# Kernel tuning notes

Hardware: AMD Instinct MI355X
Metric: run time of the kernel (lower is better)

## Reference

```python
import jax, jax.numpy as jnp
import numpy as np

T, DB, H, U, MC, MT, L, K = 16, 512, 512, 1024, 8, 4, 64, 64
Hh = H // 2


def setup_inputs() -> dict:
    key = jax.random.key(0)
    ks = jax.random.split(key, 16)
    s = 0.05
    inp = {
        'feat': jax.random.normal(ks[0], (T, DB, H), jnp.float32),
        'key': jax.random.normal(ks[1], (T, H), jnp.float32),
        'final_feature': jax.random.normal(ks[2], (T, L, H), jnp.float32),
        'Wih_f': jax.random.normal(ks[3], (3 * Hh, H), jnp.float32) * s,
        'Whh_f': jax.random.normal(ks[4], (3 * Hh, Hh), jnp.float32) * s,
        'bih_f': jnp.zeros((3 * Hh,), jnp.float32),
        'bhh_f': jnp.zeros((3 * Hh,), jnp.float32),
        'Wih_b': jax.random.normal(ks[5], (3 * Hh, H), jnp.float32) * s,
        'Whh_b': jax.random.normal(ks[6], (3 * Hh, Hh), jnp.float32) * s,
        'bih_b': jnp.zeros((3 * Hh,), jnp.float32),
        'bhh_b': jnp.zeros((3 * Hh,), jnp.float32),
        'Wb': jax.random.normal(ks[7], (H, H), jnp.float32) * s,
        'bb': jnp.zeros((H,), jnp.float32),
        'Kemb': jax.random.normal(ks[8], (K, H), jnp.float32) * s,
        'col_idx': jax.random.randint(ks[9], (U, MC), 0, DB, jnp.int32),
        'col_mask': jax.random.randint(ks[10], (U, MC), 0, 2, jnp.int32).at[:, 0].set(1),
        'tab_idx': jax.random.randint(ks[11], (U, MT), 0, DB, jnp.int32),
        'tab_mask': jax.random.randint(ks[12], (U, MT), 0, 2, jnp.int32).at[:, 0].set(1),
        'attn_mask': jax.random.randint(ks[13], (T, U), 0, 2, jnp.int32).at[:, 0].set(1),
    }
    return inp


def _gru_cell(x, h, Wih, Whh, bih, bhh):
    gi = x @ Wih.T + bih
    gh = h @ Whh.T + bhh
    ir, iz, inn = jnp.split(gi, 3, axis=-1)
    hr, hz, hn = jnp.split(gh, 3, axis=-1)
    r = jax.nn.sigmoid(ir + hr)
    z = jax.nn.sigmoid(iz + hz)
    n = jnp.tanh(inn + r * hn)
    return (1.0 - z) * n + z * h


def reference(feat, key, final_feature, Wih_f, Whh_f, bih_f, bhh_f,
              Wih_b, Whh_b, bih_b, bhh_b, Wb, bb, Kemb,
              col_idx, col_mask, tab_idx, tab_mask, attn_mask):
    # --- irregular gather + masked mean over schema-graph index groups ---
    def masked_mean(idx, m):
        g = feat[:, idx, :]                        # (T, U, M, H) gather
        mf = m.astype(feat.dtype)
        s = jnp.einsum('tumh,um->tuh', g, mf)
        cnt = jnp.maximum(mf.sum(-1), 1.0)         # (U,)
        return s / cnt[None, :, None]

    col_feat = masked_mean(col_idx, col_mask)      # (T, U, H)
    tab_feat = masked_mean(tab_idx, tab_mask)      # (T, U, H)

    # --- bidirectional GRU fuse over the 2-step [table, column] sequence ---
    x1 = tab_feat.reshape(T * U, H)
    x2 = col_feat.reshape(T * U, H)
    h0 = jnp.zeros((T * U, Hh), feat.dtype)
    f1 = _gru_cell(x1, h0, Wih_f, Whh_f, bih_f, bhh_f)
    f2 = _gru_cell(x2, f1, Wih_f, Whh_f, bih_f, bhh_f)
    b1 = _gru_cell(x2, h0, Wih_b, Whh_b, bih_b, bhh_b)
    b2 = _gru_cell(x1, b1, Wih_b, Whh_b, bih_b, bhh_b)
    o0 = jnp.concatenate([f1, b2], axis=-1)        # output at t=0
    o1 = jnp.concatenate([f2, b1], axis=-1)        # output at t=1
    db_emb = ((o0 + o1) * 0.5).reshape(T, U, H)    # mean over seq dim

    # --- attention_sum ---
    logits = jnp.einsum('th,tuh->tu', key, db_emb)
    logits = jnp.where(attn_mask == 0, jnp.asarray(-1e9, logits.dtype), logits)
    w = jax.nn.softmax(logits, axis=-1)
    attn = jnp.einsum('tu,tuh->th', w, db_emb)     # (T, H)

    # --- output_prob with bilinear feature transform ---
    feature = final_feature + attn[:, None, :]     # (T, L, H)
    ff = jnp.tanh(feature @ Wb.T + bb)
    db_prob = jnp.einsum('tlh,tuh->tlu', ff, db_emb)
    kw_prob = jnp.einsum('tlh,kh->tlk', ff, Kemb)
    out = jax.nn.log_softmax(jnp.concatenate([db_prob, kw_prob], axis=-1), axis=-1)
    return out  # (T, L, U+K)
```

## Files before the change

kernel.cpp:

```cpp
#include <hip/hip_runtime.h>
#include <math.h>

#define T_  16
#define DB2_ 512
#define H_  512
#define Hh_ 256
#define U_  1024
#define MC_ 8
#define MT_ 4
#define L_  64
#define K_  64
#define M_  (T_*U_)

#define BM 64
#define BNG 64
#define BK 64
#define S0_ (768*512)
#define S1_ (768*256)
#define WB_ (512*512)
#define KE_ (64*512)

typedef __attribute__((ext_vector_type(8))) short bf16x8;
typedef __attribute__((ext_vector_type(4))) float f32x4;

__device__ __forceinline__ float sigmoidf_(float x) {
    return 1.f / (1.f + __expf(-x));
}
__device__ __forceinline__ float tanhf_(float x) {
    const float xc = fminf(fmaxf(x, -10.f), 10.f);
    const float t = __expf(2.f * xc);
    return (t - 1.f) / (t + 1.f);
}

__device__ __forceinline__ ushort f2bf(float f) {
    union { float f; unsigned u; } v; v.f = f;
    const unsigned r = (v.u + 0x7FFFu + ((v.u >> 16) & 1u)) >> 16;
    return (ushort)r;
}
__device__ __forceinline__ float bf2f(ushort u) {
    union { unsigned u; float f; } v; v.u = ((unsigned)u) << 16; return v.f;
}

__device__ __forceinline__ void gload16(const void* g, void* l) {
    __builtin_amdgcn_global_load_lds(
        (const __attribute__((address_space(1))) void*)g,
        (__attribute__((address_space(3))) void*)l, 16, 0, 0);
}

__global__ __launch_bounds__(256) void wcvt_kernel(
    const float* __restrict__ w0, const float* __restrict__ w1,
    const float* __restrict__ w2, const float* __restrict__ w3,
    const float* __restrict__ w4, const float* __restrict__ w5,
    ushort* __restrict__ dst)
{
    const int idx = (blockIdx.x * 256 + threadIdx.x) * 4;
    const float* src; int local;
    if      (idx < S0_)                  { src = w0; local = idx; }
    else if (idx < S0_ + S1_)            { src = w1; local = idx - S0_; }
    else if (idx < 2*S0_ + S1_)          { src = w2; local = idx - S0_ - S1_; }
    else if (idx < 2*S0_ + 2*S1_)        { src = w3; local = idx - 2*S0_ - S1_; }
    else if (idx < 2*S0_ + 2*S1_ + WB_)  { src = w4; local = idx - 2*S0_ - 2*S1_; }
    else                                 { src = w5; local = idx - 2*S0_ - 2*S1_ - WB_; }
    const float4 v = *(const float4*)(src + local);
    ushort4 o; o.x = f2bf(v.x); o.y = f2bf(v.y); o.z = f2bf(v.z); o.w = f2bf(v.w);
    *(ushort4*)(dst + idx) = o;
}

__global__ __launch_bounds__(256) void meanpool_kernel(
    const float* __restrict__ feat,
    const int* __restrict__ col_idx, const int* __restrict__ col_mask,
    const int* __restrict__ tab_idx, const int* __restrict__ tab_mask,
    ushort* __restrict__ x1, ushort* __restrict__ x2)
{
    const int u = blockIdx.x;
    const int t = blockIdx.y;
    const int tid = threadIdx.x;

    int ci[MC_], cm[MC_], ti[MT_], tm[MT_];
    float cc = 0.f, tc = 0.f;
#pragma unroll
    for (int m = 0; m < MC_; ++m) { ci[m] = col_idx[u*MC_+m]; cm[m] = col_mask[u*MC_+m]; cc += (float)cm[m]; }
#pragma unroll
    for (int m = 0; m < MT_; ++m) { ti[m] = tab_idx[u*MT_+m]; tm[m] = tab_mask[u*MT_+m]; tc += (float)tm[m]; }
    const float rc = 1.f / fmaxf(cc, 1.f);
    const float rt = 1.f / fmaxf(tc, 1.f);

    const float* fb = feat + (size_t)t * DB2_ * H_;
    const int h = tid * 2;

    float acx = 0.f, acy = 0.f, atx = 0.f, aty = 0.f;
#pragma unroll
    for (int m = 0; m < MC_; ++m) if (cm[m]) {
        const float2 v = *(const float2*)(fb + (size_t)ci[m]*H_ + h);
        acx += v.x; acy += v.y;
    }
#pragma unroll
    for (int m = 0; m < MT_; ++m) if (tm[m]) {
        const float2 v = *(const float2*)(fb + (size_t)ti[m]*H_ + h);
        atx += v.x; aty += v.y;
    }
    const size_t o = ((size_t)(t*U_ + u))*H_ + h;
    ushort2 c2; c2.x = f2bf(acx*rc); c2.y = f2bf(acy*rc);
    ushort2 t2; t2.x = f2bf(atx*rt); t2.y = f2bf(aty*rt);
    *(ushort2*)(x2 + o) = c2;
    *(ushort2*)(x1 + o) = t2;
}

template<int GN>
__device__ __forceinline__ void compute_tile64(
    f32x4 (&acc)[4][2][2],
    const ushort (&As)[BM][BK], const ushort (&Bs)[192][BK],
    int lane, int wm, int wn)
{
#pragma unroll
    for (int s = 0; s < 2; ++s) {
        const int colr = (((s*4 + (lane>>4)) ^ (lane & 7)) * 8);
        bf16x8 af[2];
#pragma unroll
        for (int fm = 0; fm < 2; ++fm)
            af[fm] = *(const bf16x8*)&As[wm*32 + fm*16 + (lane&15)][colr];
#pragma unroll
        for (int g = 0; g < 3; ++g) {
            const int gi = (g == 2) ? GN : g;
#pragma unroll
            for (int fn = 0; fn < 2; ++fn) {
                const bf16x8 bv = *(const bf16x8*)&Bs[g*64 + wn*32 + fn*16 + (lane&15)][colr];
#pragma unroll
                for (int fm = 0; fm < 2; ++fm)
                    acc[gi][fm][fn] = __builtin_amdgcn_mfma_f32_16x16x32_bf16(
                        af[fm], bv, acc[gi][fm][fn], 0, 0, 0);
            }
        }
    }
}

template<bool HAS_H>
__global__ __launch_bounds__(256, 4) void gru2_kernel(
    const ushort* __restrict__ X0, const ushort* __restrict__ X1,
    const ushort* __restrict__ Hb0, const ushort* __restrict__ Hb1,
    const ushort* __restrict__ Wih0, const ushort* __restrict__ Wih1,
    const ushort* __restrict__ Whh0, const ushort* __restrict__ Whh1,
    const float* __restrict__ bih0, const float* __restrict__ bih1,
    const float* __restrict__ bhh0, const float* __restrict__ bhh1,
    ushort* __restrict__ HoutB0, ushort* __restrict__ HoutB1,
    ushort* __restrict__ emb0, ushort* __restrict__ emb1)
{
    __shared__ __align__(16) ushort As[BM][BK];
    __shared__ __align__(16) ushort Bs[192][BK];

    const int sel = blockIdx.z;
    const ushort* Xb   = sel ? X1 : X0;
    const ushort* Hb   = sel ? Hb1 : Hb0;
    const ushort* Wihb = sel ? Wih1 : Wih0;
    const ushort* Whhb = sel ? Whh1 : Whh0;
    const float*  bih  = sel ? bih1 : bih0;
    const float*  bhh  = sel ? bhh1 : bhh0;
    ushort* Hout_b = sel ? HoutB1 : HoutB0;
    ushort* emb_b  = sel ? emb1 : emb0;

    const int tid = threadIdx.x;
    const int lane = tid & 63, wid = tid >> 6;
    const int wm = wid >> 1, wn = wid & 1;

    const int flat = blockIdx.x;
    const int i8   = flat & 7;
    const int rest = flat >> 3;
    const int jb   = rest & 3;
    const int ib   = (rest >> 2) * 8 + i8;
    const int i0 = ib * BM;
    const int j0 = jb * BNG;

    const int csw  = (((lane & 7) ^ (lane >> 3)) * 8);
    const int rsub = lane >> 3;

    ushort* const ldsA0 = &As[0][0] + (size_t)wid*512;
    ushort* const ldsA1 = &As[0][0] + (size_t)(wid+4)*512;
    ushort* ldsB[6];
#pragma unroll
    for (int s = 0; s < 6; ++s) ldsB[s] = &Bs[0][0] + (size_t)(wid + 4*s)*512;

    f32x4 acc[4][2][2] = {};

    {
        const ushort* ga0 = Xb + (size_t)(i0 + wid*8     + rsub)*H_ + csw;
        const ushort* ga1 = Xb + (size_t)(i0 + (wid+4)*8 + rsub)*H_ + csw;
        const ushort* gb[6];
#pragma unroll
        for (int s = 0; s < 6; ++s) {
            const int rowB = (wid + 4*s)*8 + rsub;
            gb[s] = Wihb + (size_t)((rowB>>6)*Hh_ + j0 + (rowB&63))*H_ + csw;
        }
        for (int k0 = 0; k0 < H_; k0 += BK) {
            gload16(ga0, ldsA0);
            gload16(ga1, ldsA1);
#pragma unroll
            for (int s = 0; s < 6; ++s) gload16(gb[s], ldsB[s]);
            ga0 += BK; ga1 += BK;
#pragma unroll
            for (int s = 0; s < 6; ++s) gb[s] += BK;
            __syncthreads();
            compute_tile64<2>(acc, As, Bs, lane, wm, wn);
            __syncthreads();
        }
    }
    if (HAS_H) {
        const ushort* ga0 = Hb + (size_t)(i0 + wid*8     + rsub)*Hh_ + csw;
        const ushort* ga1 = Hb + (size_t)(i0 + (wid+4)*8 + rsub)*Hh_ + csw;
        const ushort* gb[6];
#pragma unroll
        for (int s = 0; s < 6; ++s) {
            const int rowB = (wid + 4*s)*8 + rsub;
            gb[s] = Whhb + (size_t)((rowB>>6)*Hh_ + j0 + (rowB&63))*Hh_ + csw;
        }
        for (int k0 = 0; k0 < Hh_; k0 += BK) {
            gload16(ga0, ldsA0);
            gload16(ga1, ldsA1);
#pragma unroll
            for (int s = 0; s < 6; ++s) gload16(gb[s], ldsB[s]);
            ga0 += BK; ga1 += BK;
#pragma unroll
            for (int s = 0; s < 6; ++s) gb[s] += BK;
            __syncthreads();
            compute_tile64<3>(acc, As, Bs, lane, wm, wn);
            __syncthreads();
        }
    }

#pragma unroll
    for (int fn = 0; fn < 2; ++fn) {
        const int j = j0 + wn*32 + fn*16 + (lane & 15);
        const float bri = bih[j],       brh = bhh[j];
        const float bzi = bih[Hh_ + j], bzh = bhh[Hh_ + j];
        const float bni = bih[2*Hh_+j], bnh = bhh[2*Hh_ + j];
#pragma unroll
        for (int fm = 0; fm < 2; ++fm) {
#pragma unroll
            for (int r = 0; r < 4; ++r) {
                const int i = i0 + wm*32 + fm*16 + (lane >> 4)*4 + r;
                const float xr = acc[0][fm][fn][r] + bri + brh;
                const float xz = acc[1][fm][fn][r] + bzi + bzh;
                const float xn = acc[2][fm][fn][r] + bni;
                float hn = bnh, hprev = 0.f;
                if (HAS_H) { hn += acc[3][fm][fn][r]; hprev = bf2f(Hb[(size_t)i*Hh_ + j]); }
                const float rg = sigmoidf_(xr);
                const float zg = sigmoidf_(xz);
                const float ng = tanhf_(xn + rg * hn);
                const float hp = (1.f - zg) * ng + zg * hprev;
                if (HAS_H) {
                    emb_b[(size_t)i*H_ + j] = f2bf(0.5f * (hprev + hp));
                } else {
                    Hout_b[(size_t)i*Hh_ + j] = f2bf(hp);
                }
            }
        }
    }
}

template<int NT>
__device__ __forceinline__ float block_reduce_max(float v, float* red) {
#pragma unroll
    for (int o = 32; o > 0; o >>= 1) v = fmaxf(v, __shfl_down(v, o));
    const int wid = threadIdx.x >> 6;
    if ((threadIdx.x & 63) == 0) red[wid] = v;
    __syncthreads();
    if (threadIdx.x == 0) {
        float m = red[0];
#pragma unroll
        for (int i = 1; i < NT/64; ++i) m = fmaxf(m, red[i]);
        red[0] = m;
    }
    __syncthreads();
    const float r = red[0];
    __syncthreads();
    return r;
}

template<int NT>
__device__ __forceinline__ float block_reduce_sum(float v, float* red) {
#pragma unroll
    for (int o = 32; o > 0; o >>= 1) v += __shfl_down(v, o);
    const int wid = threadIdx.x >> 6;
    if ((threadIdx.x & 63) == 0) red[wid] = v;
    __syncthreads();
    if (threadIdx.x == 0) {
        float m = red[0];
#pragma unroll
        for (int i = 1; i < NT/64; ++i) m += red[i];
        red[0] = m;
    }
    __syncthreads();
    const float r = red[0];
    __syncthreads();
    return r;
}

__global__ __launch_bounds__(256) void attn_logits_kernel(
    const ushort* __restrict__ db, const float* __restrict__ key,
    const int* __restrict__ attn_mask, float* __restrict__ alog)
{
    const int t = blockIdx.y;
    const int tid = threadIdx.x;
    const int u = blockIdx.x*64 + (tid >> 2);
    const int kq = (tid & 3) * 128;

    const bf16x8* r8 = (const bf16x8*)(db + ((size_t)t*U_ + u)*H_ + kq);
    const float* kp = key + t*H_ + kq;
    float s = 0.f;
#pragma unroll
    for (int k8 = 0; k8 < 16; ++k8) {
        const bf16x8 v = r8[k8];
#pragma unroll
        for (int j = 0; j < 8; ++j)
            s = fmaf(kp[k8*8 + j], bf2f((ushort)v[j]), s);
    }
    s += __shfl_xor(s, 1);
    s += __shfl_xor(s, 2);
    if ((tid & 3) == 0)
        alog[t*U_ + u] = attn_mask[t*U_ + u] ? s : -1e9f;
}

__global__ __launch_bounds__(512) void attn_softmax_kernel(
    const float* __restrict__ alog, float* __restrict__ aw)
{
    __shared__ float red[8];
    const int t = blockIdx.x, tid = threadIdx.x;
    const float v0 = alog[t*U_ + tid], v1 = alog[t*U_ + tid + 512];
    const float m = block_reduce_max<512>(fmaxf(v0, v1), red);
    const float e0 = __expf(v0 - m), e1 = __expf(v1 - m);
    const float s = block_reduce_sum<512>(e0 + e1, red);
    const float inv = 1.f / s;
    aw[t*U_ + tid] = e0 * inv;
    aw[t*U_ + tid + 512] = e1 * inv;
}

__global__ __launch_bounds__(512) void attn_wsum_kernel(
    const ushort* __restrict__ db, const float* __restrict__ aw,
    float* __restrict__ part)
{
    __shared__ float sred[8][64][8];
    const int t = blockIdx.y, u0 = blockIdx.x * 128;
    const int usub = threadIdx.x >> 6;
    const int h8   = threadIdx.x & 63;

    float a[8] = {};
    for (int uu = 0; uu < 16; ++uu) {
        const int u = u0 + usub*16 + uu;
        const float w = aw[t*U_ + u];
        const bf16x8 v = *(const bf16x8*)(db + ((size_t)t*U_ + u)*H_ + h8*8);
#pragma unroll
        for (int j = 0; j < 8; ++j) a[j] = fmaf(w, bf2f((ushort)v[j]), a[j]);
    }
#pragma unroll
    for (int j = 0; j < 8; ++j) sred[usub][h8][j] = a[j];
    __syncthreads();

    const int h8r = threadIdx.x >> 3;
    const int cr  = threadIdx.x & 7;
    float s = 0.f;
#pragma unroll
    for (int us = 0; us < 8; ++us) s += sred[us][h8r][cr];
    part[((size_t)blockIdx.x*T_ + t)*H_ + h8r*8 + cr] = s;
}

__global__ __launch_bounds__(256) void featcvt_kernel(
    const float* __restrict__ finf, const float* __restrict__ part,
    ushort* __restrict__ featb)
{
    const int row = blockIdx.x;
    const int t = row >> 6;
    const int h = threadIdx.x * 2;
    const float2 v = *(const float2*)(finf + (size_t)row*H_ + h);
    float ax = 0.f, ay = 0.f;
#pragma unroll
    for (int p = 0; p < 8; ++p) {
        const float2 a = *(const float2*)(part + ((size_t)p*T_ + t)*H_ + h);
        ax += a.x; ay += a.y;
    }
    ushort2 o; o.x = f2bf(v.x + ax); o.y = f2bf(v.y + ay);
    *(ushort2*)(featb + (size_t)row*H_ + h) = o;
}

__global__ __launch_bounds__(256) void ffgemm_kernel(
    const ushort* __restrict__ featb, const ushort* __restrict__ Wbb,
    const float* __restrict__ bb, ushort* __restrict__ ffb)
{
    __shared__ __align__(16) ushort As[128][BK];
    __shared__ __align__(16) ushort Bs[64][BK];

    const int tid = threadIdx.x;
    const int lane = tid & 63, wid = tid >> 6;
    const int wm = wid >> 1, wn = wid & 1;
    const int i0 = blockIdx.y * 128;
    const int j0 = blockIdx.x * 64;
    const int csw  = (((lane & 7) ^ (lane >> 3)) * 8);
    const int rsub = lane >> 3;

    f32x4 acc[4][2] = {};

    for (int k0 = 0; k0 < H_; k0 += BK) {
#pragma unroll
        for (int cc = wid; cc < 24; cc += 4) {
            if (cc < 16) {
                const ushort* g = featb + (size_t)(i0 + cc*8 + rsub)*H_ + k0 + csw;
                gload16(g, &As[0][0] + cc*512);
            } else {
                const int c = cc - 16;
                const ushort* g = Wbb + (size_t)(j0 + c*8 + rsub)*H_ + k0 + csw;
                gload16(g, &Bs[0][0] + c*512);
            }
        }
        __syncthreads();
#pragma unroll
        for (int s = 0; s < 2; ++s) {
            const int colr = (((s*4 + (lane>>4)) ^ (lane & 7)) * 8);
            bf16x8 af[4];
#pragma unroll
            for (int fm = 0; fm < 4; ++fm)
                af[fm] = *(const bf16x8*)&As[wm*64 + fm*16 + (lane&15)][colr];
#pragma unroll
            for (int fn = 0; fn < 2; ++fn) {
                const bf16x8 bv = *(const bf16x8*)&Bs[wn*32 + fn*16 + (lane&15)][colr];
#pragma unroll
                for (int fm = 0; fm < 4; ++fm)
                    acc[fm][fn] = __builtin_amdgcn_mfma_f32_16x16x32_bf16(
                        af[fm], bv, acc[fm][fn], 0, 0, 0);
            }
        }
        __syncthreads();
    }

#pragma unroll
    for (int fn = 0; fn < 2; ++fn) {
        const int j = j0 + wn*32 + fn*16 + (lane & 15);
        const float b = bb[j];
#pragma unroll
        for (int fm = 0; fm < 4; ++fm)
#pragma unroll
            for (int r = 0; r < 4; ++r) {
                const int i = i0 + wm*64 + fm*16 + (lane >> 4)*4 + r;
                ffb[(size_t)i*H_ + j] = f2bf(tanhf_(acc[fm][fn][r] + b));
            }
    }
}

__global__ __launch_bounds__(256) void logits_kernel(
    const ushort* __restrict__ ffb, const ushort* __restrict__ dbb,
    const ushort* __restrict__ Kembb, float* __restrict__ logits)
{
    __shared__ __align__(16) ushort As[64][BK];
    __shared__ __align__(16) ushort Bs[64][BK];

    const int tid = threadIdx.x;
    const int lane = tid & 63, wid = tid >> 6;
    const int t = blockIdx.y;
    const int bx = blockIdx.x;
    const bool kw = (bx == 16);
    const int csw  = (((lane & 7) ^ (lane >> 3)) * 8);
    const int rsub = lane >> 3;

    f32x4 acc[4] = {};

    for (int k0 = 0; k0 < H_; k0 += BK) {
#pragma unroll
        for (int cc = wid; cc < 16; cc += 4) {
            if (cc < 8) {
                const ushort* g = ffb + (size_t)(t*64 + cc*8 + rsub)*H_ + k0 + csw;
                gload16(g, &As[0][0] + cc*512);
            } else {
                const int rloc = (cc-8)*8 + rsub;
                const ushort* g = kw ? (Kembb + (size_t)rloc*H_ + k0 + csw)
                                     : (dbb + (size_t)(t*U_ + bx*64 + rloc)*H_ + k0 + csw);
                gload16(g, &Bs[0][0] + (cc-8)*512);
            }
        }
        __syncthreads();
#pragma unroll
        for (int s = 0; s < 2; ++s) {
            const int colr = (((s*4 + (lane>>4)) ^ (lane & 7)) * 8);
            const bf16x8 af = *(const bf16x8*)&As[wid*16 + (lane&15)][colr];
#pragma unroll
            for (int fn = 0; fn < 4; ++fn) {
                const bf16x8 bv = *(const bf16x8*)&Bs[fn*16 + (lane&15)][colr];
                acc[fn] = __builtin_amdgcn_mfma_f32_16x16x32_bf16(af, bv, acc[fn], 0, 0, 0);
            }
        }
        __syncthreads();
    }

    const int ncols = U_ + K_;
#pragma unroll
    for (int fn = 0; fn < 4; ++fn) {
        const int jg = (kw ? U_ : bx*64) + fn*16 + (lane & 15);
#pragma unroll
        for (int r = 0; r < 4; ++r) {
            const int i = t*64 + wid*16 + (lane >> 4)*4 + r;
            logits[(size_t)i*ncols + jg] = acc[fn][r];
        }
    }
}

__global__ __launch_bounds__(256) void lsm_kernel(
    const float* __restrict__ logits, float* __restrict__ out)
{
    __shared__ float sl[U_ + K_];
    __shared__ float red[4];
    const int row = blockIdx.x;
    const int tid = threadIdx.x;
    const int ncols = U_ + K_;

    float m = -3.4e38f;
    for (int idx = tid; idx < ncols; idx += 256) {
        const float v = logits[(size_t)row*ncols + idx];
        sl[idx] = v;
        m = fmaxf(m, v);
    }
    __syncthreads();
    m = block_reduce_max<256>(m, red);

    float s = 0.f;
    for (int idx = tid; idx < ncols; idx += 256) s += __expf(sl[idx] - m);
    s = block_reduce_sum<256>(s, red);
    const float lse = m + __logf(s);

    for (int idx = tid; idx < ncols; idx += 256)
        out[(size_t)row*ncols + idx] = sl[idx] - lse;
}

extern "C" void kernel_launch(void* const* d_in, const int* in_sizes, int n_in,
                              void* d_out, int out_size, void* d_ws, size_t ws_size,
                              hipStream_t stream)
{
    const float* feat  = (const float*)d_in[0];
    const float* key   = (const float*)d_in[1];
    const float* finf  = (const float*)d_in[2];
    const float* Wih_f = (const float*)d_in[3];
    const float* Whh_f = (const float*)d_in[4];
    const float* bih_f = (const float*)d_in[5];
    const float* bhh_f = (const float*)d_in[6];
    const float* Wih_b = (const float*)d_in[7];
    const float* Whh_b = (const float*)d_in[8];
    const float* bih_b = (const float*)d_in[9];
    const float* bhh_b = (const float*)d_in[10];
    const float* Wb    = (const float*)d_in[11];
    const float* bb    = (const float*)d_in[12];
    const float* Kemb  = (const float*)d_in[13];
    const int* col_idx  = (const int*)d_in[14];
    const int* col_mask = (const int*)d_in[15];
    const int* tab_idx  = (const int*)d_in[16];
    const int* tab_mask = (const int*)d_in[17];
    const int* attn_mask= (const int*)d_in[18];
    float* out = (float*)d_out;

    char* p = (char*)d_ws;
    ushort* wbf  = (ushort*)p;  p += (size_t)(2*(S0_+S1_) + WB_ + KE_)*2;
    ushort* x1b  = (ushort*)p;  p += (size_t)M_*H_*2;
    ushort* x2b  = (ushort*)p;  p += (size_t)M_*H_*2;
    ushort* f1b  = (ushort*)p;  p += (size_t)M_*Hh_*2;
    ushort* b1b  = (ushort*)p;  p += (size_t)M_*Hh_*2;
    ushort* dbb  = (ushort*)p;  p += (size_t)M_*H_*2;
    float*  alog = (float*)p;   p += (size_t)T_*U_*4;
    float*  aw   = (float*)p;   p += (size_t)T_*U_*4;
    float*  part = (float*)p;   p += (size_t)8*T_*H_*4;
    ushort* featb= (ushort*)p;  p += (size_t)T_*L_*H_*2;
    ushort* ffb  = (ushort*)p;  p += (size_t)T_*L_*H_*2;
    float*  lg   = (float*)p;   p += (size_t)T_*L_*(U_+K_)*4;

    const ushort* Wihf_b = wbf;
    const ushort* Whhf_b = wbf + S0_;
    const ushort* Wihb_b = wbf + S0_ + S1_;
    const ushort* Whhb_b = wbf + 2*S0_ + S1_;
    const ushort* Wbb    = wbf + 2*(S0_ + S1_);
    const ushort* Kembb  = wbf + 2*(S0_ + S1_) + WB_;

    wcvt_kernel<<<(2*(S0_+S1_) + WB_ + KE_)/1024, 256, 0, stream>>>(
        Wih_f, Whh_f, Wih_b, Whh_b, Wb, Kemb, wbf);

    meanpool_kernel<<<dim3(U_, T_), 256, 0, stream>>>(
        feat, col_idx, col_mask, tab_idx, tab_mask, x1b, x2b);

    dim3 gg((M_/BM)*(Hh_/BNG), 1, 2);
    gru2_kernel<false><<<gg, 256, 0, stream>>>(
        x1b, x2b, nullptr, nullptr,
        Wihf_b, Wihb_b, Whhf_b, Whhb_b, bih_f, bih_b, bhh_f, bhh_b,
        f1b, b1b, nullptr, nullptr);
    gru2_kernel<true><<<gg, 256, 0, stream>>>(
        x2b, x1b, f1b, b1b,
        Wihf_b, Wihb_b, Whhf_b, Whhb_b, bih_f, bih_b, bhh_f, bhh_b,
        nullptr, nullptr, dbb, dbb + Hh_);

    attn_logits_kernel<<<dim3(16, T_), 256, 0, stream>>>(dbb, key, attn_mask, alog);
    attn_softmax_kernel<<<T_, 512, 0, stream>>>(alog, aw);
    attn_wsum_kernel<<<dim3(8, T_), 512, 0, stream>>>(dbb, aw, part);
    featcvt_kernel<<<T_*L_, 256, 0, stream>>>(finf, part, featb);
    ffgemm_kernel<<<dim3(H_/64, (T_*L_)/128), 256, 0, stream>>>(featb, Wbb, bb, ffb);
    logits_kernel<<<dim3(17, T_), 256, 0, stream>>>(ffb, dbb, Kembb, lg);
    lsm_kernel<<<T_*L_, 256, 0, stream>>>(lg, out);
}
```

Baseline: 256.3 us.

## Double-buffer LDS tiles in GRU GEMM to overlap global loads with MFMA

The GRU GEMM kernel now keeps two LDS buffers for the A and B tiles and issues the next k-tile's direct-to-LDS loads before computing on the current one. Partial vmcnt waits let compute overlap the in-flight loads, and the prefetch runs across the boundary between the input-weight and hidden-weight loops. LDS use doubles, so launch_bounds drops from 4 to 2 blocks per SM, which lowers occupancy in exchange for latency hiding.

Result: no change. 258.2 us (+0.8%).

```diff
diff --git a/kernel.cpp b/kernel.cpp
--- a/kernel.cpp
+++ b/kernel.cpp
@@ -106,6 +106,22 @@
     *(ushort2*)(x1 + o) = t2;
 }
 
+__device__ __forceinline__ void stage8(
+    ushort* asb, ushort* bsb, int wid,
+    const ushort* a0, const ushort* a1,
+    const ushort* b0, const ushort* b1, const ushort* b2,
+    const ushort* b3, const ushort* b4, const ushort* b5)
+{
+    gload16(a0, asb + (size_t)wid*512);
+    gload16(a1, asb + (size_t)(wid+4)*512);
+    gload16(b0, bsb + (size_t)(wid     )*512);
+    gload16(b1, bsb + (size_t)(wid +  4)*512);
+    gload16(b2, bsb + (size_t)(wid +  8)*512);
+    gload16(b3, bsb + (size_t)(wid + 12)*512);
+    gload16(b4, bsb + (size_t)(wid + 16)*512);
+    gload16(b5, bsb + (size_t)(wid + 20)*512);
+}
+
 template<int GN>
 __device__ __forceinline__ void compute_tile64(
     f32x4 (&acc)[4][2][2],
@@ -135,7 +151,7 @@
 }
 
 template<bool HAS_H>
-__global__ __launch_bounds__(256, 4) void gru2_kernel(
+__global__ __launch_bounds__(256, 2) void gru2_kernel(
     const ushort* __restrict__ X0, const ushort* __restrict__ X1,
     const ushort* __restrict__ Hb0, const ushort* __restrict__ Hb1,
     const ushort* __restrict__ Wih0, const ushort* __restrict__ Wih1,
@@ -145,8 +161,8 @@
     ushort* __restrict__ HoutB0, ushort* __restrict__ HoutB1,
     ushort* __restrict__ emb0, ushort* __restrict__ emb1)
 {
-    __shared__ __align__(16) ushort As[BM][BK];
-    __shared__ __align__(16) ushort Bs[192][BK];
+    __shared__ __align__(16) ushort As[2][BM][BK];
+    __shared__ __align__(16) ushort Bs[2][192][BK];
 
     const int sel = blockIdx.z;
     const ushort* Xb   = sel ? X1 : X0;
@@ -173,56 +189,73 @@
     const int csw  = (((lane & 7) ^ (lane >> 3)) * 8);
     const int rsub = lane >> 3;
 
-    ushort* const ldsA0 = &As[0][0] + (size_t)wid*512;
-    ushort* const ldsA1 = &As[0][0] + (size_t)(wid+4)*512;
-    ushort* ldsB[6];
-#pragma unroll
-    for (int s = 0; s < 6; ++s) ldsB[s] = &Bs[0][0] + (size_t)(wid + 4*s)*512;
-
-    f32x4 acc[4][2][2] = {};
-
-    {
-        const ushort* ga0 = Xb + (size_t)(i0 + wid*8     + rsub)*H_ + csw;
-        const ushort* ga1 = Xb + (size_t)(i0 + (wid+4)*8 + rsub)*H_ + csw;
-        const ushort* gb[6];
+    const ushort* xa0 = Xb + (size_t)(i0 + wid*8     + rsub)*H_ + csw;
+    const ushort* xa1 = Xb + (size_t)(i0 + (wid+4)*8 + rsub)*H_ + csw;
+    const ushort* xb[6];
+#pragma unroll
+    for (int s = 0; s < 6; ++s) {
+        const int rowB = (wid + 4*s)*8 + rsub;
+        xb[s] = Wihb + (size_t)((rowB>>6)*Hh_ + j0 + (rowB&63))*H_ + csw;
+    }
+    const ushort* ha0 = nullptr; const ushort* ha1 = nullptr;
+    const ushort* hb[6] = {};
+    if (HAS_H) {
+        ha0 = Hb + (size_t)(i0 + wid*8     + rsub)*Hh_ + csw;
+        ha1 = Hb + (size_t)(i0 + (wid+4)*8 + rsub)*Hh_ + csw;
 #pragma unroll
         for (int s = 0; s < 6; ++s) {
             const int rowB = (wid + 4*s)*8 + rsub;
-            gb[s] = Wihb + (size_t)((rowB>>6)*Hh_ + j0 + (rowB&63))*H_ + csw;
-        }
-        for (int k0 = 0; k0 < H_; k0 += BK) {
-            gload16(ga0, ldsA0);
-            gload16(ga1, ldsA1);
-#pragma unroll
-            for (int s = 0; s < 6; ++s) gload16(gb[s], ldsB[s]);
-            ga0 += BK; ga1 += BK;
-#pragma unroll
-            for (int s = 0; s < 6; ++s) gb[s] += BK;
-            __syncthreads();
-            compute_tile64<2>(acc, As, Bs, lane, wm, wn);
-            __syncthreads();
-        }
+            hb[s] = Whhb + (size_t)((rowB>>6)*Hh_ + j0 + (rowB&63))*Hh_ + csw;
+        }
+    }
+
+    f32x4 acc[4][2][2] = {};
+
+    const int NK1 = H_ / BK;
+    const int NK2 = Hh_ / BK;
+    int cur = 0;
+
+    stage8(&As[0][0][0], &Bs[0][0][0], wid, xa0, xa1,
+           xb[0], xb[1], xb[2], xb[3], xb[4], xb[5]);
+
+    for (int k = 1; k <= NK1; ++k) {
+        if (k < NK1) {
+            xa0 += BK; xa1 += BK;
+#pragma unroll
+            for (int s = 0; s < 6; ++s) xb[s] += BK;
+            stage8(&As[cur^1][0][0], &Bs[cur^1][0][0], wid, xa0, xa1,
+                   xb[0], xb[1], xb[2], xb[3], xb[4], xb[5]);
+            asm volatile("s_waitcnt vmcnt(8)" ::: "memory");
+        } else if (HAS_H) {
+            stage8(&As[cur^1][0][0], &Bs[cur^1][0][0], wid, ha0, ha1,
+                   hb[0], hb[1], hb[2], hb[3], hb[4], hb[5]);
+            asm volatile("s_waitcnt vmcnt(8)" ::: "memory");
+        } else {
+            asm volatile("s_waitcnt vmcnt(0)" ::: "memory");
+        }
+        __builtin_amdgcn_s_barrier();
+        __builtin_amdgcn_sched_barrier(0);
+        compute_tile64<2>(acc, As[cur], Bs[cur], lane, wm, wn);
+        __builtin_amdgcn_s_barrier();
+        cur ^= 1;
     }
     if (HAS_H) {
-        const ushort* ga0 = Hb + (size_t)(i0 + wid*8     + rsub)*Hh_ + csw;
-        const ushort* ga1 = Hb + (size_t)(i0 + (wid+4)*8 + rsub)*Hh_ + csw;
-        const ushort* gb[6];
-#pragma unroll
-        for (int s = 0; s < 6; ++s) {
-            const int rowB = (wid + 4*s)*8 + rsub;
-            gb[s] = Whhb + (size_t)((rowB>>6)*Hh_ + j0 + (rowB&63))*Hh_ + csw;
-        }
-        for (int k0 = 0; k0 < Hh_; k0 += BK) {
-            gload16(ga0, ldsA0);
-            gload16(ga1, ldsA1);
-#pragma unroll
-            for (int s = 0; s < 6; ++s) gload16(gb[s], ldsB[s]);
-            ga0 += BK; ga1 += BK;
-#pragma unroll
-            for (int s = 0; s < 6; ++s) gb[s] += BK;
-            __syncthreads();
-            compute_tile64<3>(acc, As, Bs, lane, wm, wn);
-            __syncthreads();
+        for (int k = 1; k <= NK2; ++k) {
+            if (k < NK2) {
+                ha0 += BK; ha1 += BK;
+#pragma unroll
+                for (int s = 0; s < 6; ++s) hb[s] += BK;
+                stage8(&As[cur^1][0][0], &Bs[cur^1][0][0], wid, ha0, ha1,
+                       hb[0], hb[1], hb[2], hb[3], hb[4], hb[5]);
+                asm volatile("s_waitcnt vmcnt(8)" ::: "memory");
+            } else {
+                asm volatile("s_waitcnt vmcnt(0)" ::: "memory");
+            }
+            __builtin_amdgcn_s_barrier();
+            __builtin_amdgcn_sched_barrier(0);
+            compute_tile64<3>(acc, As[cur], Bs[cur], lane, wm, wn);
+            __builtin_amdgcn_s_barrier();
+            cur ^= 1;
         }
     }
 
```
